# Kernel optimization log

Hardware: AMD Instinct MI355X
Metric: run time of the kernel (lower is better)

Reference implementation:

```python
import jax, jax.numpy as jnp
import numpy as np

D_MODEL = 1024
HEADS = 4
HDIM = 64


def setup_inputs() -> dict:
    key = jax.random.key(0)
    k_x, k_qw, k_qb, k_kw, k_kb, k_hw = jax.random.split(key, 6)
    hidden_states = jax.random.normal(k_x, (2, 4096, D_MODEL), dtype=jnp.float32)
    # xavier_uniform bound for Linear(d_model -> heads*hdim)
    fan_out = HEADS * HDIM
    bound = float(np.sqrt(6.0 / (D_MODEL + fan_out)))
    q_weight = jax.random.uniform(k_qw, (fan_out, D_MODEL), minval=-bound, maxval=bound, dtype=jnp.float32)
    k_weight = jax.random.uniform(k_kw, (fan_out, D_MODEL), minval=-bound, maxval=bound, dtype=jnp.float32)
    # nn.Linear default bias init: U(-1/sqrt(fan_in), 1/sqrt(fan_in))
    b_bound = float(1.0 / np.sqrt(D_MODEL))
    q_bias = jax.random.uniform(k_qb, (fan_out,), minval=-b_bound, maxval=b_bound, dtype=jnp.float32)
    k_bias = jax.random.uniform(k_kb, (fan_out,), minval=-b_bound, maxval=b_bound, dtype=jnp.float32)
    indexer_weights = jax.random.normal(k_hw, (HEADS,), dtype=jnp.float32) * 0.1
    return {
        "hidden_states": hidden_states,
        "q_weight": q_weight,
        "q_bias": q_bias,
        "k_weight": k_weight,
        "k_bias": k_bias,
        "indexer_weights": indexer_weights,
    }


def reference(hidden_states, q_weight, q_bias, k_weight, k_bias, indexer_weights):
    b, s, _ = hidden_states.shape
    # Linear projections: x @ W^T + b  -> [b, s, heads*hdim]
    q = hidden_states @ q_weight.T + q_bias
    k = hidden_states @ k_weight.T + k_bias
    q = q.reshape(b, s, HEADS, HDIM)  # [b, s, h, d]
    k = k.reshape(b, s, HEADS, HDIM)
    # per-head QK^T -> [b, h, s, s]
    scores = jnp.einsum("bqhd,bkhd->bhqk", q, k)
    scores = jax.nn.relu(scores)
    # weighted sum over heads -> [b, s, s]
    index_scores = jnp.einsum("bhqk,h->bqk", scores, indexer_weights)
    return index_scores
```

## Files before the change

### kernel.cpp

```cpp
#include <hip/hip_runtime.h>


typedef __bf16 bf16;
typedef __bf16 bf16x4 __attribute__((ext_vector_type(4)));
typedef __bf16 bf16x8 __attribute__((ext_vector_type(8)));
typedef float f32x4 __attribute__((ext_vector_type(4)));

#define NB 2
#define SEQ 4096
#define DMODEL 1024
#define NHEAD 4
#define HDIM 64
#define NPROJ 256
#define MTOT 8192

__device__ __forceinline__ void async16(const void* g, void* l) {
  __builtin_amdgcn_global_load_lds(
      (const __attribute__((address_space(1))) void*)g,
      (__attribute__((address_space(3))) void*)l, 16, 0, 0);
}

__global__ __launch_bounds__(256) void k_convert(const float* __restrict__ wq,
                                                 const float* __restrict__ wk,
                                                 bf16* __restrict__ wqb,
                                                 bf16* __restrict__ wkb) {
  int i = blockIdx.x * 256 + threadIdx.x;
  float4 a = ((const float4*)wq)[i];
  bf16x4 oa = {(bf16)a.x, (bf16)a.y, (bf16)a.z, (bf16)a.w};
  ((bf16x4*)wqb)[i] = oa;
  float4 b = ((const float4*)wk)[i];
  bf16x4 ob = {(bf16)b.x, (bf16)b.y, (bf16)b.z, (bf16)b.w};
  ((bf16x4*)wkb)[i] = ob;
}

__global__ __launch_bounds__(256, 4) void k_proj(
    const float* __restrict__ x, const bf16* __restrict__ wqb,
    const bf16* __restrict__ wkb, const float* __restrict__ qbias,
    const float* __restrict__ kbias, bf16* __restrict__ Qb,
    bf16* __restrict__ Kb) {
  __shared__ __align__(16) bf16 As[64 * 72];
  __shared__ __align__(16) bf16 Bs[128 * 64];
  const int t = threadIdx.x;
  const int lane = t & 63, w = t >> 6;
  const int m16 = lane & 15, q = lane >> 4;
  const int m0 = blockIdx.x * 64;
  const int z = blockIdx.y;
  const int nh = blockIdx.z;
  const bf16* __restrict__ W = z ? wkb : wqb;

  f32x4 acc[4][2];
#pragma unroll
  for (int i = 0; i < 4; i++)
#pragma unroll
    for (int j = 0; j < 2; j++) acc[i][j] = {0.f, 0.f, 0.f, 0.f};

  for (int kt = 0; kt < 16; kt++) {
#pragma unroll
    for (int p = 0; p < 4; p++) {
      int n0 = w * 32 + p * 8;
      int r = n0 + (lane >> 3);
      int c = (lane & 7) ^ (r & 7);
      async16(W + (size_t)(nh * 128 + r) * DMODEL + kt * 64 + c * 8,
              Bs + n0 * 64);
    }
#pragma unroll
    for (int p = 0; p < 4; p++) {
      int r = p * 16 + (t >> 4);
      int c = (t & 15) * 4;
      float4 v = *(const float4*)(x + (size_t)(m0 + r) * DMODEL + kt * 64 + c);
      bf16x4 o = {(bf16)v.x, (bf16)v.y, (bf16)v.z, (bf16)v.w};
      *(bf16x4*)(As + r * 72 + c) = o;
    }
    __builtin_amdgcn_s_waitcnt(0);
    __syncthreads();

#pragma unroll
    for (int s = 0; s < 2; s++) {
      bf16x8 a[4], b[2];
#pragma unroll
      for (int mt = 0; mt < 4; mt++)
        a[mt] = *(const bf16x8*)(As + (mt * 16 + m16) * 72 + s * 32 + q * 8);
#pragma unroll
      for (int nt = 0; nt < 2; nt++) {
        int n = w * 32 + nt * 16 + m16;
        int cc = (4 * s + q) ^ (n & 7);
        b[nt] = *(const bf16x8*)(Bs + n * 64 + cc * 8);
      }
#pragma unroll
      for (int mt = 0; mt < 4; mt++)
#pragma unroll
        for (int nt = 0; nt < 2; nt++)
          acc[mt][nt] = __builtin_amdgcn_mfma_f32_16x16x32_bf16(
              a[mt], b[nt], acc[mt][nt], 0, 0, 0);
    }
    __syncthreads();
  }

  const float* __restrict__ bias = z ? kbias : qbias;
  bf16* __restrict__ outp = z ? Kb : Qb;
#pragma unroll
  for (int nt = 0; nt < 2; nt++) {
    int col = nh * 128 + w * 32 + nt * 16 + m16;
    float bv = bias[col];
#pragma unroll
    for (int mt = 0; mt < 4; mt++) {
      int row0 = m0 + mt * 16 + q * 4;
#pragma unroll
      for (int e = 0; e < 4; e++)
        outp[(size_t)(row0 + e) * NPROJ + col] = (bf16)(acc[mt][nt][e] + bv);
    }
  }
}

__global__ __launch_bounds__(256, 2) void k_scores(
    const bf16* __restrict__ Qb, const bf16* __restrict__ Kb,
    const float* __restrict__ iw, float* __restrict__ out) {
  __shared__ __align__(16) bf16 Ks[128 * 256];
  const int t = threadIdx.x;
  const int lane = t & 63, w = t >> 6;
  const int m16 = lane & 15, q = lane >> 4;

  const int bx = blockIdx.x;
  const int kq = bx & 7;
  const int strip = bx >> 3;
  const int bz = strip >> 5;
  const int q0 = (strip & 31) * 128;

  const float wh0 = iw[0], wh1 = iw[1], wh2 = iw[2], wh3 = iw[3];
  const float whs[4] = {wh0, wh1, wh2, wh3};

  bf16x8 aq[2][4][2];
  {
    const bf16* qp =
        Qb + (size_t)(bz * SEQ + q0 + w * 32 + m16) * NPROJ + q * 8;
#pragma unroll
    for (int mt = 0; mt < 2; mt++)
#pragma unroll
      for (int h = 0; h < 4; h++)
#pragma unroll
        for (int j = 0; j < 2; j++)
          aq[mt][h][j] =
              *(const bf16x8*)(qp + (size_t)mt * 16 * NPROJ + h * 64 + j * 32);
  }

  for (int i = 0; i < 4; i++) {
    const int kx = kq * 4 + i;
    const size_t kbase = ((size_t)bz * SEQ + (size_t)kx * 128) * NPROJ;
    __syncthreads();
#pragma unroll
    for (int p = 0; p < 16; p++) {
      int g = w * 16 + p;
      int r = g * 2 + (lane >> 5);
      int c = (lane & 31) ^ (r & 31);
      async16(Kb + kbase + (size_t)r * NPROJ + c * 8, Ks + g * 512);
    }
    __builtin_amdgcn_s_waitcnt(0);
    __syncthreads();

    f32x4 accf[2][8];
#pragma unroll
    for (int mt = 0; mt < 2; mt++)
#pragma unroll
      for (int nt = 0; nt < 8; nt++) accf[mt][nt] = {0.f, 0.f, 0.f, 0.f};

#pragma unroll
    for (int h = 0; h < 4; h++) {
      const float wh = whs[h];
      bf16x8 bk[8][2];
#pragma unroll
      for (int nt = 0; nt < 8; nt++) {
        int n = nt * 16 + m16;
        const bf16* kb_ = Ks + (size_t)n * 256;
        int c0 = (h * 8 + q) ^ (n & 31);
        int c1 = (h * 8 + 4 + q) ^ (n & 31);
        bk[nt][0] = *(const bf16x8*)(kb_ + c0 * 8);
        bk[nt][1] = *(const bf16x8*)(kb_ + c1 * 8);
      }
#pragma unroll
      for (int mt = 0; mt < 2; mt++)
#pragma unroll
        for (int nt = 0; nt < 8; nt++) {
          f32x4 tacc = {0.f, 0.f, 0.f, 0.f};
          tacc = __builtin_amdgcn_mfma_f32_16x16x32_bf16(aq[mt][h][0], bk[nt][0],
                                                         tacc, 0, 0, 0);
          tacc = __builtin_amdgcn_mfma_f32_16x16x32_bf16(aq[mt][h][1], bk[nt][1],
                                                         tacc, 0, 0, 0);
#pragma unroll
          for (int e = 0; e < 4; e++)
            accf[mt][nt][e] += wh * fmaxf(tacc[e], 0.f);
        }
    }

#pragma unroll
    for (int mt = 0; mt < 2; mt++)
#pragma unroll
      for (int e = 0; e < 4; e++) {
        int r = q0 + w * 32 + mt * 16 + q * 4 + e;
        size_t ob = ((size_t)bz * SEQ + r) * SEQ + (size_t)kx * 128;
#pragma unroll
        for (int nt = 0; nt < 8; nt++)
          out[ob + nt * 16 + m16] = accf[mt][nt][e];
      }
  }
}

extern "C" void kernel_launch(void* const* d_in, const int* in_sizes, int n_in,
                              void* d_out, int out_size, void* d_ws, size_t ws_size,
                              hipStream_t stream) {
  const float* x  = (const float*)d_in[0];
  const float* wq = (const float*)d_in[1];
  const float* qb = (const float*)d_in[2];
  const float* wk = (const float*)d_in[3];
  const float* kb = (const float*)d_in[4];
  const float* iw = (const float*)d_in[5];
  float* out = (float*)d_out;

  char* ws = (char*)d_ws;
  bf16* wqb = (bf16*)ws;
  bf16* wkb = (bf16*)(ws + 524288);
  bf16* Qb  = (bf16*)(ws + 1048576);
  bf16* Kb  = (bf16*)(ws + 1048576 + 4194304);

  k_convert<<<256, 256, 0, stream>>>(wq, wk, wqb, wkb);
  k_proj<<<dim3(128, 2, 2), 256, 0, stream>>>(x, wqb, wkb, qb, kb, Qb, Kb);
  k_scores<<<512, 256, 0, stream>>>(Qb, Kb, iw, out);
}
```

Before: 196.1 us.

## Double-buffer proj and scores stages, pre-convert x, transpose score tiles for vector stores

Adds a full conversion of x to bf16, staged in the output buffer as scratch, so the projection kernel loads both operands with async global-to-LDS copies. The projection kernel now double-buffers its LDS tiles and computes all 256 output columns per block, with vectorized bias and output stores. The scores kernel streams K in double-buffered 64-row chunks and swaps the MFMA operand order, so each lane holds contiguous columns and can issue 16-byte nontemporal stores instead of scalar ones. The aim is to overlap loads with MFMA work and to cut output store transactions. In exchange it adds an extra pass over x and lowers projection occupancy to one block per CU, with far fewer projection blocks.

```diff
diff --git a/kernel.cpp b/kernel.cpp
--- a/kernel.cpp
+++ b/kernel.cpp
@@ -6,11 +6,8 @@
 typedef __bf16 bf16x8 __attribute__((ext_vector_type(8)));
 typedef float f32x4 __attribute__((ext_vector_type(4)));
 
-#define NB 2
 #define SEQ 4096
 #define DMODEL 1024
-#define NHEAD 4
-#define HDIM 64
 #define NPROJ 256
 #define MTOT 8192
 
@@ -20,94 +17,119 @@
       (__attribute__((address_space(3))) void*)l, 16, 0, 0);
 }
 
-__global__ __launch_bounds__(256) void k_convert(const float* __restrict__ wq,
+__global__ __launch_bounds__(256) void k_convert(const float* __restrict__ x,
+                                                 const float* __restrict__ wq,
                                                  const float* __restrict__ wk,
+                                                 bf16* __restrict__ xb,
                                                  bf16* __restrict__ wqb,
                                                  bf16* __restrict__ wkb) {
-  int i = blockIdx.x * 256 + threadIdx.x;
-  float4 a = ((const float4*)wq)[i];
-  bf16x4 oa = {(bf16)a.x, (bf16)a.y, (bf16)a.z, (bf16)a.w};
-  ((bf16x4*)wqb)[i] = oa;
-  float4 b = ((const float4*)wk)[i];
-  bf16x4 ob = {(bf16)b.x, (bf16)b.y, (bf16)b.z, (bf16)b.w};
-  ((bf16x4*)wkb)[i] = ob;
-}
-
-__global__ __launch_bounds__(256, 4) void k_proj(
-    const float* __restrict__ x, const bf16* __restrict__ wqb,
+  const int b = blockIdx.x, t = threadIdx.x;
+  if (b < 2048) {
+    int i = b * 256 + t;
+#pragma unroll
+    for (int r = 0; r < 4; r++) {
+      float4 v = ((const float4*)x)[i + r * 524288];
+      bf16x4 o = {(bf16)v.x, (bf16)v.y, (bf16)v.z, (bf16)v.w};
+      ((bf16x4*)xb)[i + r * 524288] = o;
+    }
+  } else {
+    int i = (b - 2048) * 256 + t;
+#pragma unroll
+    for (int r = 0; r < 2; r++) {
+      float4 a = ((const float4*)wq)[i + r * 32768];
+      bf16x4 oa = {(bf16)a.x, (bf16)a.y, (bf16)a.z, (bf16)a.w};
+      ((bf16x4*)wqb)[i + r * 32768] = oa;
+      float4 c = ((const float4*)wk)[i + r * 32768];
+      bf16x4 oc = {(bf16)c.x, (bf16)c.y, (bf16)c.z, (bf16)c.w};
+      ((bf16x4*)wkb)[i + r * 32768] = oc;
+    }
+  }
+}
+
+__global__ __launch_bounds__(256, 1) void k_proj(
+    const bf16* __restrict__ xb, const bf16* __restrict__ wqb,
     const bf16* __restrict__ wkb, const float* __restrict__ qbias,
     const float* __restrict__ kbias, bf16* __restrict__ Qb,
     bf16* __restrict__ Kb) {
-  __shared__ __align__(16) bf16 As[64 * 72];
-  __shared__ __align__(16) bf16 Bs[128 * 64];
+  __shared__ __align__(16) bf16 As[2][64 * 64];
+  __shared__ __align__(16) bf16 Bs[2][256 * 64];
   const int t = threadIdx.x;
   const int lane = t & 63, w = t >> 6;
   const int m16 = lane & 15, q = lane >> 4;
   const int m0 = blockIdx.x * 64;
   const int z = blockIdx.y;
-  const int nh = blockIdx.z;
   const bf16* __restrict__ W = z ? wkb : wqb;
 
-  f32x4 acc[4][2];
-#pragma unroll
-  for (int i = 0; i < 4; i++)
-#pragma unroll
-    for (int j = 0; j < 2; j++) acc[i][j] = {0.f, 0.f, 0.f, 0.f};
+  f32x4 acc[4][4];
+#pragma unroll
+  for (int nt = 0; nt < 4; nt++)
+#pragma unroll
+    for (int mt = 0; mt < 4; mt++) acc[nt][mt] = {0.f, 0.f, 0.f, 0.f};
+
+  auto stage = [&](int buf, int kt) {
+#pragma unroll
+    for (int p = 0; p < 2; p++) {
+      int g = w * 2 + p;
+      int r = g * 8 + (lane >> 3);
+      int c = (lane & 7) ^ (r & 7);
+      async16(xb + (size_t)(m0 + r) * DMODEL + kt * 64 + c * 8,
+              As[buf] + g * 512);
+    }
+#pragma unroll
+    for (int p = 0; p < 8; p++) {
+      int g = w * 8 + p;
+      int r = g * 8 + (lane >> 3);
+      int c = (lane & 7) ^ (r & 7);
+      async16(W + (size_t)r * DMODEL + kt * 64 + c * 8, Bs[buf] + g * 512);
+    }
+  };
+
+  stage(0, 0);
+  __builtin_amdgcn_s_waitcnt(0);
+  __syncthreads();
 
   for (int kt = 0; kt < 16; kt++) {
-#pragma unroll
-    for (int p = 0; p < 4; p++) {
-      int n0 = w * 32 + p * 8;
-      int r = n0 + (lane >> 3);
-      int c = (lane & 7) ^ (r & 7);
-      async16(W + (size_t)(nh * 128 + r) * DMODEL + kt * 64 + c * 8,
-              Bs + n0 * 64);
-    }
-#pragma unroll
-    for (int p = 0; p < 4; p++) {
-      int r = p * 16 + (t >> 4);
-      int c = (t & 15) * 4;
-      float4 v = *(const float4*)(x + (size_t)(m0 + r) * DMODEL + kt * 64 + c);
-      bf16x4 o = {(bf16)v.x, (bf16)v.y, (bf16)v.z, (bf16)v.w};
-      *(bf16x4*)(As + r * 72 + c) = o;
+    if (kt < 15) stage((kt + 1) & 1, kt + 1);
+    const bf16* As_ = As[kt & 1];
+    const bf16* Bs_ = Bs[kt & 1];
+#pragma unroll
+    for (int s = 0; s < 2; s++) {
+      bf16x8 af[4], bx[4];
+#pragma unroll
+      for (int nt = 0; nt < 4; nt++) {
+        int n = w * 64 + nt * 16 + m16;
+        int cc = (s * 4 + q) ^ (n & 7);
+        af[nt] = *(const bf16x8*)(Bs_ + n * 64 + cc * 8);
+      }
+#pragma unroll
+      for (int mt = 0; mt < 4; mt++) {
+        int m = mt * 16 + m16;
+        int cc = (s * 4 + q) ^ (m & 7);
+        bx[mt] = *(const bf16x8*)(As_ + m * 64 + cc * 8);
+      }
+#pragma unroll
+      for (int nt = 0; nt < 4; nt++)
+#pragma unroll
+        for (int mt = 0; mt < 4; mt++)
+          acc[nt][mt] = __builtin_amdgcn_mfma_f32_16x16x32_bf16(
+              af[nt], bx[mt], acc[nt][mt], 0, 0, 0);
     }
     __builtin_amdgcn_s_waitcnt(0);
     __syncthreads();
-
-#pragma unroll
-    for (int s = 0; s < 2; s++) {
-      bf16x8 a[4], b[2];
-#pragma unroll
-      for (int mt = 0; mt < 4; mt++)
-        a[mt] = *(const bf16x8*)(As + (mt * 16 + m16) * 72 + s * 32 + q * 8);
-#pragma unroll
-      for (int nt = 0; nt < 2; nt++) {
-        int n = w * 32 + nt * 16 + m16;
-        int cc = (4 * s + q) ^ (n & 7);
-        b[nt] = *(const bf16x8*)(Bs + n * 64 + cc * 8);
-      }
-#pragma unroll
-      for (int mt = 0; mt < 4; mt++)
-#pragma unroll
-        for (int nt = 0; nt < 2; nt++)
-          acc[mt][nt] = __builtin_amdgcn_mfma_f32_16x16x32_bf16(
-              a[mt], b[nt], acc[mt][nt], 0, 0, 0);
-    }
-    __syncthreads();
   }
 
   const float* __restrict__ bias = z ? kbias : qbias;
   bf16* __restrict__ outp = z ? Kb : Qb;
 #pragma unroll
-  for (int nt = 0; nt < 2; nt++) {
-    int col = nh * 128 + w * 32 + nt * 16 + m16;
-    float bv = bias[col];
+  for (int nt = 0; nt < 4; nt++) {
+    int n0 = w * 64 + nt * 16 + q * 4;
+    float4 bv = *(const float4*)(bias + n0);
 #pragma unroll
     for (int mt = 0; mt < 4; mt++) {
-      int row0 = m0 + mt * 16 + q * 4;
-#pragma unroll
-      for (int e = 0; e < 4; e++)
-        outp[(size_t)(row0 + e) * NPROJ + col] = (bf16)(acc[mt][nt][e] + bv);
+      int m = m0 + mt * 16 + m16;
+      bf16x4 o = {(bf16)(acc[nt][mt][0] + bv.x), (bf16)(acc[nt][mt][1] + bv.y),
+                  (bf16)(acc[nt][mt][2] + bv.z), (bf16)(acc[nt][mt][3] + bv.w)};
+      *(bf16x4*)(outp + (size_t)m * NPROJ + n0) = o;
     }
   }
 }
@@ -115,7 +137,7 @@
 __global__ __launch_bounds__(256, 2) void k_scores(
     const bf16* __restrict__ Qb, const bf16* __restrict__ Kb,
     const float* __restrict__ iw, float* __restrict__ out) {
-  __shared__ __align__(16) bf16 Ks[128 * 256];
+  __shared__ __align__(16) bf16 Ks[2][64 * 256];
   const int t = threadIdx.x;
   const int lane = t & 63, w = t >> 6;
   const int m16 = lane & 15, q = lane >> 4;
@@ -125,82 +147,91 @@
   const int strip = bx >> 3;
   const int bz = strip >> 5;
   const int q0 = (strip & 31) * 128;
-
-  const float wh0 = iw[0], wh1 = iw[1], wh2 = iw[2], wh3 = iw[3];
-  const float whs[4] = {wh0, wh1, wh2, wh3};
+  const int k0 = kq * 512;
+
+  const float whs[4] = {iw[0], iw[1], iw[2], iw[3]};
 
   bf16x8 aq[2][4][2];
   {
     const bf16* qp =
         Qb + (size_t)(bz * SEQ + q0 + w * 32 + m16) * NPROJ + q * 8;
 #pragma unroll
-    for (int mt = 0; mt < 2; mt++)
+    for (int qt = 0; qt < 2; qt++)
 #pragma unroll
       for (int h = 0; h < 4; h++)
 #pragma unroll
         for (int j = 0; j < 2; j++)
-          aq[mt][h][j] =
-              *(const bf16x8*)(qp + (size_t)mt * 16 * NPROJ + h * 64 + j * 32);
-  }
-
-  for (int i = 0; i < 4; i++) {
-    const int kx = kq * 4 + i;
-    const size_t kbase = ((size_t)bz * SEQ + (size_t)kx * 128) * NPROJ;
-    __syncthreads();
-#pragma unroll
-    for (int p = 0; p < 16; p++) {
-      int g = w * 16 + p;
+          aq[qt][h][j] = *(const bf16x8*)(qp + (size_t)qt * 16 * NPROJ +
+                                          h * 64 + j * 32);
+  }
+
+  auto stage = [&](int buf, int st) {
+#pragma unroll
+    for (int p = 0; p < 8; p++) {
+      int g = w * 8 + p;
       int r = g * 2 + (lane >> 5);
       int c = (lane & 31) ^ (r & 31);
-      async16(Kb + kbase + (size_t)r * NPROJ + c * 8, Ks + g * 512);
-    }
+      async16(Kb + ((size_t)bz * SEQ + k0 + st * 64 + r) * NPROJ + c * 8,
+              Ks[buf] + g * 512);
+    }
+  };
+
+  stage(0, 0);
+  __builtin_amdgcn_s_waitcnt(0);
+  __syncthreads();
+
+  for (int st = 0; st < 8; st++) {
+    if (st < 7) stage((st + 1) & 1, st + 1);
+    const bf16* KsB = Ks[st & 1];
+
+    f32x4 accf[4][2];
+#pragma unroll
+    for (int kt = 0; kt < 4; kt++)
+#pragma unroll
+      for (int qt = 0; qt < 2; qt++) accf[kt][qt] = {0.f, 0.f, 0.f, 0.f};
+
+#pragma unroll
+    for (int h = 0; h < 4; h++) {
+      const float wh = whs[h];
+      bf16x8 ak[4][2];
+#pragma unroll
+      for (int kt = 0; kt < 4; kt++) {
+        int r = kt * 16 + m16;
+        const bf16* kp = KsB + r * 256;
+        int c0 = (h * 8 + q) ^ (r & 31);
+        int c1 = (h * 8 + 4 + q) ^ (r & 31);
+        ak[kt][0] = *(const bf16x8*)(kp + c0 * 8);
+        ak[kt][1] = *(const bf16x8*)(kp + c1 * 8);
+      }
+#pragma unroll
+      for (int kt = 0; kt < 4; kt++)
+#pragma unroll
+        for (int qt = 0; qt < 2; qt++) {
+          f32x4 tacc = {0.f, 0.f, 0.f, 0.f};
+          tacc = __builtin_amdgcn_mfma_f32_16x16x32_bf16(ak[kt][0],
+                                                         aq[qt][h][0], tacc,
+                                                         0, 0, 0);
+          tacc = __builtin_amdgcn_mfma_f32_16x16x32_bf16(ak[kt][1],
+                                                         aq[qt][h][1], tacc,
+                                                         0, 0, 0);
+#pragma unroll
+          for (int e = 0; e < 4; e++)
+            accf[kt][qt][e] += wh * fmaxf(tacc[e], 0.f);
+        }
+    }
+
     __builtin_amdgcn_s_waitcnt(0);
     __syncthreads();
 
-    f32x4 accf[2][8];
-#pragma unroll
-    for (int mt = 0; mt < 2; mt++)
-#pragma unroll
-      for (int nt = 0; nt < 8; nt++) accf[mt][nt] = {0.f, 0.f, 0.f, 0.f};
-
-#pragma unroll
-    for (int h = 0; h < 4; h++) {
-      const float wh = whs[h];
-      bf16x8 bk[8][2];
-#pragma unroll
-      for (int nt = 0; nt < 8; nt++) {
-        int n = nt * 16 + m16;
-        const bf16* kb_ = Ks + (size_t)n * 256;
-        int c0 = (h * 8 + q) ^ (n & 31);
-        int c1 = (h * 8 + 4 + q) ^ (n & 31);
-        bk[nt][0] = *(const bf16x8*)(kb_ + c0 * 8);
-        bk[nt][1] = *(const bf16x8*)(kb_ + c1 * 8);
-      }
-#pragma unroll
-      for (int mt = 0; mt < 2; mt++)
-#pragma unroll
-        for (int nt = 0; nt < 8; nt++) {
-          f32x4 tacc = {0.f, 0.f, 0.f, 0.f};
-          tacc = __builtin_amdgcn_mfma_f32_16x16x32_bf16(aq[mt][h][0], bk[nt][0],
-                                                         tacc, 0, 0, 0);
-          tacc = __builtin_amdgcn_mfma_f32_16x16x32_bf16(aq[mt][h][1], bk[nt][1],
-                                                         tacc, 0, 0, 0);
-#pragma unroll
-          for (int e = 0; e < 4; e++)
-            accf[mt][nt][e] += wh * fmaxf(tacc[e], 0.f);
-        }
-    }
-
-#pragma unroll
-    for (int mt = 0; mt < 2; mt++)
-#pragma unroll
-      for (int e = 0; e < 4; e++) {
-        int r = q0 + w * 32 + mt * 16 + q * 4 + e;
-        size_t ob = ((size_t)bz * SEQ + r) * SEQ + (size_t)kx * 128;
-#pragma unroll
-        for (int nt = 0; nt < 8; nt++)
-          out[ob + nt * 16 + m16] = accf[mt][nt][e];
-      }
+#pragma unroll
+    for (int qt = 0; qt < 2; qt++) {
+      size_t rb = ((size_t)bz * SEQ + q0 + w * 32 + qt * 16 + m16) * SEQ;
+#pragma unroll
+      for (int kt = 0; kt < 4; kt++) {
+        int col = k0 + st * 64 + kt * 16 + q * 4;
+        __builtin_nontemporal_store(accf[kt][qt], (f32x4*)(out + rb + col));
+      }
+    }
   }
 }
 
@@ -220,8 +251,9 @@
   bf16* wkb = (bf16*)(ws + 524288);
   bf16* Qb  = (bf16*)(ws + 1048576);
   bf16* Kb  = (bf16*)(ws + 1048576 + 4194304);
-
-  k_convert<<<256, 256, 0, stream>>>(wq, wk, wqb, wkb);
-  k_proj<<<dim3(128, 2, 2), 256, 0, stream>>>(x, wqb, wkb, qb, kb, Qb, Kb);
+  bf16* xb  = (bf16*)d_out;
+
+  k_convert<<<2176, 256, 0, stream>>>(x, wq, wk, xb, wqb, wkb);
+  k_proj<<<dim3(128, 2), 256, 0, stream>>>(xb, wqb, wkb, qb, kb, Qb, Kb);
   k_scores<<<512, 256, 0, stream>>>(Qb, Kb, iw, out);
 }
```

New measurement: 212.0 us. 8.1% more time.
